# Performance work log

Hardware: AMD Instinct MI355X
Metric: run time of the kernel (lower is better)

Reference implementation:

```python
import jax, jax.numpy as jnp
import numpy as np

WIN = 9        # window_size from init
EPS = 1e-05    # eps from init


def _box_sum(x, win):
    """Depthwise 3D conv with a ones kernel (local box sum), SAME padding."""
    c = x.shape[1]
    kernel = jnp.ones((c, 1, win, win, win), dtype=x.dtype)
    pad = win // 2
    return jax.lax.conv_general_dilated(
        x, kernel,
        window_strides=(1, 1, 1),
        padding=[(pad, pad)] * 3,
        dimension_numbers=('NCDHW', 'OIDHW', 'NCDHW'),
        feature_group_count=c,
    )


def setup_inputs() -> dict:
    key = jax.random.key(0)
    k1, k2 = jax.random.split(key)
    shape = (2, 1, 160, 160, 160)  # (B, C, H, W, D)
    return {
        'y_true': jax.random.normal(k1, shape, dtype=jnp.float32),
        'y_pred': jax.random.normal(k2, shape, dtype=jnp.float32),
    }


def reference(y_true, y_pred):
    window_volume = float(WIN ** 3)  # 729
    y_true_mean = _box_sum(y_true, WIN) / (window_volume + EPS)
    y_pred_mean = _box_sum(y_pred, WIN) / (window_volume + EPS)
    td = y_true - y_true_mean
    pd = y_pred - y_pred_mean
    y_true_var = _box_sum(td * td, WIN)
    y_pred_var = _box_sum(pd * pd, WIN)
    cross = _box_sum(td * pd, WIN)
    cc = cross / jnp.sqrt((y_true_var + EPS) * (y_pred_var + EPS))
    return -jnp.mean(cc)
```

## Files before the change

kernel.cpp:

```cpp
#include <hip/hip_runtime.h>
#include <math.h>

namespace {

constexpr int BB = 2;
constexpr int HH = 160;
constexpr int WW = 160;
constexpr int DD = 160;
constexpr int NV = BB * HH * WW * DD;
constexpr float WVOL = 729.0f;
constexpr float EPSF = 1e-5f;

constexpr int SLICE = WW * DD;

constexpr int Wt = 16, Dt = 16;
constexpr int WH = Wt + 8;
constexpr int DH = Dt + 8;
constexpr int Hseg = 40;
constexpr int NWT = WW / Wt;
constexpr int NDT = DD / Dt;
constexpr int NHS = HH / Hseg;
constexpr int NBLK = BB * NHS * NWT * NDT;

__global__ __launch_bounds__(256) void pa_mean(const float* __restrict__ t,
                                               const float* __restrict__ p,
                                               float* __restrict__ mt,
                                               float* __restrict__ mp) {
    __shared__ float sT[WH * DH], sP[WH * DH];
    __shared__ float dT[WH * Dt], dP[WH * Dt];
    int bid = blockIdx.x;
    int dt_ = bid % NDT; int r = bid / NDT;
    int wt_ = r % NWT;   r /= NWT;
    int hs  = r % NHS;   int b = r / NHS;
    int w0 = wt_ * Wt, d0 = dt_ * Dt, h0 = hs * Hseg;
    int tw = threadIdx.x >> 4, td = threadIdx.x & 15;
    const float* tB = t + (size_t)b * HH * SLICE;
    const float* pB = p + (size_t)b * HH * SLICE;
    float rT[9], rP[9];
#pragma unroll
    for (int m = 0; m < 9; ++m) { rT[m] = 0.f; rP[m] = 0.f; }

    for (int j = h0 - 4; j < h0 + Hseg + 4; ++j) {
        bool jok = (unsigned)j < (unsigned)HH;
        for (int li = threadIdx.x; li < WH * DH; li += 256) {
            int lw = li / DH, ld = li - lw * DH;
            int gw = w0 - 4 + lw, gd = d0 - 4 + ld;
            float vt = 0.f, vp = 0.f;
            if (jok && (unsigned)gw < (unsigned)WW && (unsigned)gd < (unsigned)DD) {
                int g = j * SLICE + gw * DD + gd;
                vt = tB[g]; vp = pB[g];
            }
            sT[li] = vt; sP[li] = vp;
        }
        __syncthreads();
        for (int li = threadIdx.x; li < WH * Dt; li += 256) {
            int lw = li >> 4, ld = li & 15;
            const float* r1 = &sT[lw * DH + ld];
            const float* r2 = &sP[lw * DH + ld];
            float s1 = 0.f, s2 = 0.f;
#pragma unroll
            for (int m = 0; m < 9; ++m) { s1 += r1[m]; s2 += r2[m]; }
            dT[li] = s1; dP[li] = s2;
        }
        __syncthreads();
        float s1 = 0.f, s2 = 0.f;
#pragma unroll
        for (int m = 0; m < 9; ++m) { s1 += dT[(tw + m) * Dt + td]; s2 += dP[(tw + m) * Dt + td]; }
#pragma unroll
        for (int m = 0; m < 8; ++m) { rT[m] = rT[m + 1]; rP[m] = rP[m + 1]; }
        rT[8] = s1; rP[8] = s2;
        int h = j - 4;
        if (h >= h0) {
            float a = 0.f, c = 0.f;
#pragma unroll
            for (int m = 0; m < 9; ++m) { a += rT[m]; c += rP[m]; }
            int g = (b * HH + h) * SLICE + (w0 + tw) * DD + (d0 + td);
            mt[g] = a / WVOL; mp[g] = c / WVOL;
        }
        __syncthreads();
    }
}

__global__ __launch_bounds__(256) void pb_cc(const float* __restrict__ t,
                                             const float* __restrict__ p,
                                             const float* __restrict__ mt,
                                             const float* __restrict__ mp,
                                             double* __restrict__ partials) {
    __shared__ float qA[WH * DH], qB[WH * DH], qC[WH * DH];
    __shared__ float dA[WH * Dt], dB[WH * Dt], dC[WH * Dt];
    int bid = blockIdx.x;
    int dt_ = bid % NDT; int r = bid / NDT;
    int wt_ = r % NWT;   r /= NWT;
    int hs  = r % NHS;   int b = r / NHS;
    int w0 = wt_ * Wt, d0 = dt_ * Dt, h0 = hs * Hseg;
    int tw = threadIdx.x >> 4, td = threadIdx.x & 15;
    size_t boff = (size_t)b * HH * SLICE;
    const float* tB = t + boff;
    const float* pB = p + boff;
    const float* uB = mt + boff;
    const float* vB = mp + boff;
    float rA[9], rB[9], rC[9];
#pragma unroll
    for (int m = 0; m < 9; ++m) { rA[m] = 0.f; rB[m] = 0.f; rC[m] = 0.f; }
    double acc = 0.0;

    for (int j = h0 - 4; j < h0 + Hseg + 4; ++j) {
        bool jok = (unsigned)j < (unsigned)HH;
        for (int li = threadIdx.x; li < WH * DH; li += 256) {
            int lw = li / DH, ld = li - lw * DH;
            int gw = w0 - 4 + lw, gd = d0 - 4 + ld;
            float av = 0.f, bv = 0.f, cv = 0.f;
            if (jok && (unsigned)gw < (unsigned)WW && (unsigned)gd < (unsigned)DD) {
                int g = j * SLICE + gw * DD + gd;
                float tdv = tB[g] - uB[g];
                float pdv = pB[g] - vB[g];
                av = tdv * tdv; bv = pdv * pdv; cv = tdv * pdv;
            }
            qA[li] = av; qB[li] = bv; qC[li] = cv;
        }
        __syncthreads();
        for (int li = threadIdx.x; li < WH * Dt; li += 256) {
            int lw = li >> 4, ld = li & 15;
            const float* r1 = &qA[lw * DH + ld];
            const float* r2 = &qB[lw * DH + ld];
            const float* r3 = &qC[lw * DH + ld];
            float s1 = 0.f, s2 = 0.f, s3 = 0.f;
#pragma unroll
            for (int m = 0; m < 9; ++m) { s1 += r1[m]; s2 += r2[m]; s3 += r3[m]; }
            dA[li] = s1; dB[li] = s2; dC[li] = s3;
        }
        __syncthreads();
        float s1 = 0.f, s2 = 0.f, s3 = 0.f;
#pragma unroll
        for (int m = 0; m < 9; ++m) {
            int o = (tw + m) * Dt + td;
            s1 += dA[o]; s2 += dB[o]; s3 += dC[o];
        }
#pragma unroll
        for (int m = 0; m < 8; ++m) { rA[m] = rA[m + 1]; rB[m] = rB[m + 1]; rC[m] = rC[m + 1]; }
        rA[8] = s1; rB[8] = s2; rC[8] = s3;
        int h = j - 4;
        if (h >= h0) {
            float sa = 0.f, sb = 0.f, sc = 0.f;
#pragma unroll
            for (int m = 0; m < 9; ++m) { sa += rA[m]; sb += rB[m]; sc += rC[m]; }
            float cc = sc / sqrtf((sa + EPSF) * (sb + EPSF));
            acc += (double)cc;
        }
        __syncthreads();
    }

#pragma unroll
    for (int off = 32; off > 0; off >>= 1)
        acc += __shfl_down(acc, off, 64);
    __shared__ double red[4];
    int lane = threadIdx.x & 63;
    int wv = threadIdx.x >> 6;
    if (lane == 0) red[wv] = acc;
    __syncthreads();
    if (threadIdx.x == 0)
        partials[blockIdx.x] = red[0] + red[1] + red[2] + red[3];
}

__global__ void k7_reduce(const double* __restrict__ partials, float* __restrict__ out) {
    __shared__ double red[256];
    double s = 0.0;
    for (int i = threadIdx.x; i < NBLK; i += 256)
        s += partials[i];
    red[threadIdx.x] = s;
    __syncthreads();
    for (int ofs = 128; ofs > 0; ofs >>= 1) {
        if (threadIdx.x < ofs) red[threadIdx.x] += red[threadIdx.x + ofs];
        __syncthreads();
    }
    if (threadIdx.x == 0)
        out[0] = -(float)(red[0] / (double)NV);
}

}

extern "C" void kernel_launch(void* const* d_in, const int* in_sizes, int n_in,
                              void* d_out, int out_size, void* d_ws, size_t ws_size,
                              hipStream_t stream) {
    const float* t = (const float*)d_in[0];
    const float* p = (const float*)d_in[1];
    float* out = (float*)d_out;

    char* ws = (char*)d_ws;
    double* partials = (double*)ws;
    float* mt = (float*)(ws + 16384);
    float* mp = mt + NV;

    pa_mean<<<NBLK, 256, 0, stream>>>(t, p, mt, mp);
    pb_cc<<<NBLK, 256, 0, stream>>>(t, p, mt, mp, partials);
    k7_reduce<<<1, 256, 0, stream>>>(partials, out);
}
```

Measured before the change: 318.8 us.

## Vectorize box-sum kernels with float4 tiles and store deviations instead of means

Both stencil kernels now work on float4 vectors along D. Each thread computes four outputs with a sliding 9-tap sum over three adjacent float4 values, and the tiles become 32 wide in W with 20-slice H segments. The first kernel now writes the deviations t-mean and p-mean, so the second kernel reads two fields instead of four. This cuts global traffic and gives wider loads, at the cost of more registers for the float4 ring buffers, which may lower occupancy, and more halo overhead per H segment.

```diff
diff --git a/kernel.cpp b/kernel.cpp
--- a/kernel.cpp
+++ b/kernel.cpp
@@ -11,141 +11,172 @@
 constexpr float WVOL = 729.0f;
 constexpr float EPSF = 1e-5f;
 
-constexpr int SLICE = WW * DD;
-
-constexpr int Wt = 16, Dt = 16;
-constexpr int WH = Wt + 8;
-constexpr int DH = Dt + 8;
-constexpr int Hseg = 40;
+constexpr int SLICE4 = WW * DD / 4;
+constexpr int FIELD4 = HH * SLICE4;
+
+constexpr int Wt = 32, Qt = 8;
+constexpr int WHs = Wt + 8;
+constexpr int QHs = Qt + 2;
+constexpr int SSTR = 11;
+constexpr int DSTR = 9;
+constexpr int Hseg = 20;
+constexpr int NHS = HH / Hseg;
 constexpr int NWT = WW / Wt;
-constexpr int NDT = DD / Dt;
-constexpr int NHS = HH / Hseg;
-constexpr int NBLK = BB * NHS * NWT * NDT;
-
-__global__ __launch_bounds__(256) void pa_mean(const float* __restrict__ t,
-                                               const float* __restrict__ p,
-                                               float* __restrict__ mt,
-                                               float* __restrict__ mp) {
-    __shared__ float sT[WH * DH], sP[WH * DH];
-    __shared__ float dT[WH * Dt], dP[WH * Dt];
-    int bid = blockIdx.x;
-    int dt_ = bid % NDT; int r = bid / NDT;
-    int wt_ = r % NWT;   r /= NWT;
-    int hs  = r % NHS;   int b = r / NHS;
-    int w0 = wt_ * Wt, d0 = dt_ * Dt, h0 = hs * Hseg;
-    int tw = threadIdx.x >> 4, td = threadIdx.x & 15;
-    const float* tB = t + (size_t)b * HH * SLICE;
-    const float* pB = p + (size_t)b * HH * SLICE;
-    float rT[9], rP[9];
-#pragma unroll
-    for (int m = 0; m < 9; ++m) { rT[m] = 0.f; rP[m] = 0.f; }
+constexpr int NQT = DD / (4 * Qt);
+constexpr int NTILE = NWT * NQT;
+constexpr int NSEG = BB * NHS;
+constexpr int NBLK = NTILE * NSEG;
+
+__device__ __forceinline__ float4 f4z() { return make_float4(0.f, 0.f, 0.f, 0.f); }
+
+__device__ __forceinline__ float4 slide9q(const float4 a, const float4 b, const float4 c) {
+    float f[12] = {a.x, a.y, a.z, a.w, b.x, b.y, b.z, b.w, c.x, c.y, c.z, c.w};
+    float s0 = 0.f, s1 = 0.f, s2 = 0.f, s3 = 0.f;
+#pragma unroll
+    for (int m = 0; m < 9; ++m) {
+        s0 += f[m]; s1 += f[m + 1]; s2 += f[m + 2]; s3 += f[m + 3];
+    }
+    return make_float4(s0, s1, s2, s3);
+}
+
+__device__ __forceinline__ void addq(float4& s, const float4 v) {
+    s.x += v.x; s.y += v.y; s.z += v.z; s.w += v.w;
+}
+
+__device__ __forceinline__ void decode(int bid, int& b, int& h0, int& w0, int& q0) {
+    int k = bid >> 4;
+    int s = bid & 15;
+    b = s >> 3;
+    h0 = (s & 7) * Hseg;
+    w0 = (k / NQT) * Wt;
+    q0 = (k % NQT) * Qt;
+}
+
+__global__ __launch_bounds__(256) void pa_td(const float4* __restrict__ t,
+                                             const float4* __restrict__ p,
+                                             float4* __restrict__ TD,
+                                             float4* __restrict__ PD) {
+    __shared__ float4 sT[WHs * SSTR], sP[WHs * SSTR];
+    __shared__ float4 dT[WHs * DSTR], dP[WHs * DSTR];
+    int b, h0, w0, q0;
+    decode(blockIdx.x, b, h0, w0, q0);
+    int tw = threadIdx.x >> 3, tq = threadIdx.x & 7;
+    const float4* tB = t + (size_t)b * FIELD4;
+    const float4* pB = p + (size_t)b * FIELD4;
+    float4* TDb = TD + (size_t)b * FIELD4;
+    float4* PDb = PD + (size_t)b * FIELD4;
+
+    float4 rT[9], rP[9];
+#pragma unroll
+    for (int m = 0; m < 9; ++m) { rT[m] = f4z(); rP[m] = f4z(); }
 
     for (int j = h0 - 4; j < h0 + Hseg + 4; ++j) {
         bool jok = (unsigned)j < (unsigned)HH;
-        for (int li = threadIdx.x; li < WH * DH; li += 256) {
-            int lw = li / DH, ld = li - lw * DH;
-            int gw = w0 - 4 + lw, gd = d0 - 4 + ld;
-            float vt = 0.f, vp = 0.f;
-            if (jok && (unsigned)gw < (unsigned)WW && (unsigned)gd < (unsigned)DD) {
-                int g = j * SLICE + gw * DD + gd;
+        for (int li = threadIdx.x; li < WHs * QHs; li += 256) {
+            int lw = li / QHs, lq = li - lw * QHs;
+            int gw = w0 - 4 + lw, gq = q0 - 1 + lq;
+            float4 vt = f4z(), vp = f4z();
+            if (jok && (unsigned)gw < (unsigned)WW && (unsigned)gq < (unsigned)(DD / 4)) {
+                int g = j * SLICE4 + gw * (DD / 4) + gq;
                 vt = tB[g]; vp = pB[g];
             }
-            sT[li] = vt; sP[li] = vp;
-        }
-        __syncthreads();
-        for (int li = threadIdx.x; li < WH * Dt; li += 256) {
-            int lw = li >> 4, ld = li & 15;
-            const float* r1 = &sT[lw * DH + ld];
-            const float* r2 = &sP[lw * DH + ld];
-            float s1 = 0.f, s2 = 0.f;
-#pragma unroll
-            for (int m = 0; m < 9; ++m) { s1 += r1[m]; s2 += r2[m]; }
-            dT[li] = s1; dP[li] = s2;
-        }
-        __syncthreads();
-        float s1 = 0.f, s2 = 0.f;
-#pragma unroll
-        for (int m = 0; m < 9; ++m) { s1 += dT[(tw + m) * Dt + td]; s2 += dP[(tw + m) * Dt + td]; }
+            sT[lw * SSTR + lq] = vt; sP[lw * SSTR + lq] = vp;
+        }
+        __syncthreads();
+        for (int li = threadIdx.x; li < WHs * Qt; li += 256) {
+            int lw = li >> 3, lq = li & 7;
+            int o = lw * SSTR + lq;
+            dT[lw * DSTR + lq] = slide9q(sT[o], sT[o + 1], sT[o + 2]);
+            dP[lw * DSTR + lq] = slide9q(sP[o], sP[o + 1], sP[o + 2]);
+        }
+        __syncthreads();
+        float4 s1 = f4z(), s2 = f4z();
+#pragma unroll
+        for (int m = 0; m < 9; ++m) {
+            addq(s1, dT[(tw + m) * DSTR + tq]);
+            addq(s2, dP[(tw + m) * DSTR + tq]);
+        }
 #pragma unroll
         for (int m = 0; m < 8; ++m) { rT[m] = rT[m + 1]; rP[m] = rP[m + 1]; }
         rT[8] = s1; rP[8] = s2;
         int h = j - 4;
         if (h >= h0) {
-            float a = 0.f, c = 0.f;
-#pragma unroll
-            for (int m = 0; m < 9; ++m) { a += rT[m]; c += rP[m]; }
-            int g = (b * HH + h) * SLICE + (w0 + tw) * DD + (d0 + td);
-            mt[g] = a / WVOL; mp[g] = c / WVOL;
-        }
-        __syncthreads();
-    }
-}
-
-__global__ __launch_bounds__(256) void pb_cc(const float* __restrict__ t,
-                                             const float* __restrict__ p,
-                                             const float* __restrict__ mt,
-                                             const float* __restrict__ mp,
+            float4 a = f4z(), c = f4z();
+#pragma unroll
+            for (int m = 0; m < 9; ++m) { addq(a, rT[m]); addq(c, rP[m]); }
+            int g = h * SLICE4 + (w0 + tw) * (DD / 4) + (q0 + tq);
+            float4 tv = tB[g], pv = pB[g];
+            float4 td4, pd4;
+            td4.x = tv.x - a.x / WVOL; td4.y = tv.y - a.y / WVOL;
+            td4.z = tv.z - a.z / WVOL; td4.w = tv.w - a.w / WVOL;
+            pd4.x = pv.x - c.x / WVOL; pd4.y = pv.y - c.y / WVOL;
+            pd4.z = pv.z - c.z / WVOL; pd4.w = pv.w - c.w / WVOL;
+            TDb[g] = td4; PDb[g] = pd4;
+        }
+        __syncthreads();
+    }
+}
+
+__global__ __launch_bounds__(256) void pb_cc(const float4* __restrict__ TD,
+                                             const float4* __restrict__ PD,
                                              double* __restrict__ partials) {
-    __shared__ float qA[WH * DH], qB[WH * DH], qC[WH * DH];
-    __shared__ float dA[WH * Dt], dB[WH * Dt], dC[WH * Dt];
-    int bid = blockIdx.x;
-    int dt_ = bid % NDT; int r = bid / NDT;
-    int wt_ = r % NWT;   r /= NWT;
-    int hs  = r % NHS;   int b = r / NHS;
-    int w0 = wt_ * Wt, d0 = dt_ * Dt, h0 = hs * Hseg;
-    int tw = threadIdx.x >> 4, td = threadIdx.x & 15;
-    size_t boff = (size_t)b * HH * SLICE;
-    const float* tB = t + boff;
-    const float* pB = p + boff;
-    const float* uB = mt + boff;
-    const float* vB = mp + boff;
-    float rA[9], rB[9], rC[9];
-#pragma unroll
-    for (int m = 0; m < 9; ++m) { rA[m] = 0.f; rB[m] = 0.f; rC[m] = 0.f; }
+    __shared__ float4 sA[WHs * SSTR], sB[WHs * SSTR], sC[WHs * SSTR];
+    __shared__ float4 dA[WHs * DSTR], dB[WHs * DSTR], dC[WHs * DSTR];
+    int b, h0, w0, q0;
+    decode(blockIdx.x, b, h0, w0, q0);
+    int tw = threadIdx.x >> 3, tq = threadIdx.x & 7;
+    const float4* tdB = TD + (size_t)b * FIELD4;
+    const float4* pdB = PD + (size_t)b * FIELD4;
+
+    float4 rA[9], rB[9], rC[9];
+#pragma unroll
+    for (int m = 0; m < 9; ++m) { rA[m] = f4z(); rB[m] = f4z(); rC[m] = f4z(); }
     double acc = 0.0;
 
     for (int j = h0 - 4; j < h0 + Hseg + 4; ++j) {
         bool jok = (unsigned)j < (unsigned)HH;
-        for (int li = threadIdx.x; li < WH * DH; li += 256) {
-            int lw = li / DH, ld = li - lw * DH;
-            int gw = w0 - 4 + lw, gd = d0 - 4 + ld;
-            float av = 0.f, bv = 0.f, cv = 0.f;
-            if (jok && (unsigned)gw < (unsigned)WW && (unsigned)gd < (unsigned)DD) {
-                int g = j * SLICE + gw * DD + gd;
-                float tdv = tB[g] - uB[g];
-                float pdv = pB[g] - vB[g];
-                av = tdv * tdv; bv = pdv * pdv; cv = tdv * pdv;
+        for (int li = threadIdx.x; li < WHs * QHs; li += 256) {
+            int lw = li / QHs, lq = li - lw * QHs;
+            int gw = w0 - 4 + lw, gq = q0 - 1 + lq;
+            float4 qa = f4z(), qb = f4z(), qc = f4z();
+            if (jok && (unsigned)gw < (unsigned)WW && (unsigned)gq < (unsigned)(DD / 4)) {
+                int g = j * SLICE4 + gw * (DD / 4) + gq;
+                float4 td4 = tdB[g], pd4 = pdB[g];
+                qa.x = td4.x * td4.x; qa.y = td4.y * td4.y; qa.z = td4.z * td4.z; qa.w = td4.w * td4.w;
+                qb.x = pd4.x * pd4.x; qb.y = pd4.y * pd4.y; qb.z = pd4.z * pd4.z; qb.w = pd4.w * pd4.w;
+                qc.x = td4.x * pd4.x; qc.y = td4.y * pd4.y; qc.z = td4.z * pd4.z; qc.w = td4.w * pd4.w;
             }
-            qA[li] = av; qB[li] = bv; qC[li] = cv;
-        }
-        __syncthreads();
-        for (int li = threadIdx.x; li < WH * Dt; li += 256) {
-            int lw = li >> 4, ld = li & 15;
-            const float* r1 = &qA[lw * DH + ld];
-            const float* r2 = &qB[lw * DH + ld];
-            const float* r3 = &qC[lw * DH + ld];
-            float s1 = 0.f, s2 = 0.f, s3 = 0.f;
-#pragma unroll
-            for (int m = 0; m < 9; ++m) { s1 += r1[m]; s2 += r2[m]; s3 += r3[m]; }
-            dA[li] = s1; dB[li] = s2; dC[li] = s3;
-        }
-        __syncthreads();
-        float s1 = 0.f, s2 = 0.f, s3 = 0.f;
+            int o = lw * SSTR + lq;
+            sA[o] = qa; sB[o] = qb; sC[o] = qc;
+        }
+        __syncthreads();
+        for (int li = threadIdx.x; li < WHs * Qt; li += 256) {
+            int lw = li >> 3, lq = li & 7;
+            int o = lw * SSTR + lq, od = lw * DSTR + lq;
+            dA[od] = slide9q(sA[o], sA[o + 1], sA[o + 2]);
+            dB[od] = slide9q(sB[o], sB[o + 1], sB[o + 2]);
+            dC[od] = slide9q(sC[o], sC[o + 1], sC[o + 2]);
+        }
+        __syncthreads();
+        float4 s1 = f4z(), s2 = f4z(), s3 = f4z();
 #pragma unroll
         for (int m = 0; m < 9; ++m) {
-            int o = (tw + m) * Dt + td;
-            s1 += dA[o]; s2 += dB[o]; s3 += dC[o];
+            int o = (tw + m) * DSTR + tq;
+            addq(s1, dA[o]); addq(s2, dB[o]); addq(s3, dC[o]);
         }
 #pragma unroll
         for (int m = 0; m < 8; ++m) { rA[m] = rA[m + 1]; rB[m] = rB[m + 1]; rC[m] = rC[m + 1]; }
         rA[8] = s1; rB[8] = s2; rC[8] = s3;
         int h = j - 4;
         if (h >= h0) {
-            float sa = 0.f, sb = 0.f, sc = 0.f;
-#pragma unroll
-            for (int m = 0; m < 9; ++m) { sa += rA[m]; sb += rB[m]; sc += rC[m]; }
-            float cc = sc / sqrtf((sa + EPSF) * (sb + EPSF));
-            acc += (double)cc;
+            float4 sa = f4z(), sb = f4z(), sc = f4z();
+#pragma unroll
+            for (int m = 0; m < 9; ++m) { addq(sa, rA[m]); addq(sb, rB[m]); addq(sc, rC[m]); }
+            float c0 = sc.x / sqrtf((sa.x + EPSF) * (sb.x + EPSF));
+            float c1 = sc.y / sqrtf((sa.y + EPSF) * (sb.y + EPSF));
+            float c2 = sc.z / sqrtf((sa.z + EPSF) * (sb.z + EPSF));
+            float c3 = sc.w / sqrtf((sa.w + EPSF) * (sb.w + EPSF));
+            acc += (double)c0 + (double)c1 + (double)c2 + (double)c3;
         }
         __syncthreads();
     }
@@ -182,16 +213,16 @@
 extern "C" void kernel_launch(void* const* d_in, const int* in_sizes, int n_in,
                               void* d_out, int out_size, void* d_ws, size_t ws_size,
                               hipStream_t stream) {
-    const float* t = (const float*)d_in[0];
-    const float* p = (const float*)d_in[1];
+    const float4* t = (const float4*)d_in[0];
+    const float4* p = (const float4*)d_in[1];
     float* out = (float*)d_out;
 
     char* ws = (char*)d_ws;
     double* partials = (double*)ws;
-    float* mt = (float*)(ws + 16384);
-    float* mp = mt + NV;
-
-    pa_mean<<<NBLK, 256, 0, stream>>>(t, p, mt, mp);
-    pb_cc<<<NBLK, 256, 0, stream>>>(t, p, mt, mp, partials);
+    float4* TD = (float4*)(ws + 16384);
+    float4* PD = TD + (NV / 4);
+
+    pa_td<<<NBLK, 256, 0, stream>>>(t, p, TD, PD);
+    pb_cc<<<NBLK, 256, 0, stream>>>(TD, PD, partials);
     k7_reduce<<<1, 256, 0, stream>>>(partials, out);
 }
```

Result: faster. 290.0 us (-9.1%).
